# Performance work log

Hardware: AMD Instinct MI355X
Metric: run time of the kernel (lower is better)

## Reference

```python
import jax, jax.numpy as jnp
import numpy as np

N_IN, N_OUT, N_HID = 4, 3, 64
N = N_OUT + N_HID  # 67 neurons (outputs first, matching neuron_key2idx ordering)
H, W = 1024, 1024


def setup_inputs() -> dict:
    key = jax.random.key(0)
    ks = jax.random.split(key, 6)
    inputs = jax.random.normal(ks[0], (H, W, N_IN), jnp.float32)
    # sparse NEAT connectivity encoded as masked dense matrices
    m_in = (jax.random.uniform(ks[1], (N_IN, N)) < 0.5).astype(jnp.float32)
    m_rec = (jax.random.uniform(ks[2], (N, N)) < 0.25).astype(jnp.float32)
    W_in = jax.random.normal(ks[3], (N_IN, N), jnp.float32) * m_in
    W_rec = jax.random.normal(ks[4], (N, N), jnp.float32) * 0.3 * m_rec
    bias = jax.random.normal(ks[5], (N,), jnp.float32) * 0.1
    response = jnp.ones((N,), jnp.float32)
    # neurons with no incoming connections output exactly 0 (original code path)
    has_in = ((m_in.sum(0) + m_rec.sum(0)) > 0).astype(jnp.float32)
    return {"inputs": inputs, "W_in": W_in, "W_rec": W_rec, "bias": bias,
            "response": response, "has_in": has_in, "n_passes": 2}


def reference(inputs, W_in, W_rec, bias, response, has_in, n_passes):
    lead = inputs.shape[:-1]
    x = inputs.reshape(-1, inputs.shape[-1])  # [B, N_IN]
    activs = jnp.zeros((x.shape[0], bias.shape[0]), x.dtype)  # [B, N]
    for _ in range(n_passes):  # small fixed recurrent pass count
        # sum-aggregation of weighted incoming edges from inputs and prev activs
        agg = x @ W_in + activs @ W_rec  # [B, N]
        activs = has_in * jnp.tanh(bias + response * agg)
    out = activs[:, :N_OUT]
    return out.reshape(lead + (N_OUT,))
```

## Files before the change

### kernel.cpp

```cpp
#include <hip/hip_runtime.h>

#define NN   67
#define NOUT 3
#define NIN  4
#define PKW  16
#define PK_FLOATS (NN * PKW)
#define PK_BYTES  (PK_FLOATS * 4)
#define C2   2.885390081777927f

typedef float v2f __attribute__((ext_vector_type(2)));

__device__ __forceinline__ v2f vfma(v2f a, v2f b, v2f c) {
    return __builtin_elementwise_fma(a, b, c);
}

__device__ __forceinline__ float fexp2(float x) {
    float r; asm("v_exp_f32 %0, %1" : "=v"(r) : "v"(x)); return r;
}
__device__ __forceinline__ float frcp(float x) {
    float r; asm("v_rcp_f32 %0, %1" : "=v"(r) : "v"(x)); return r;
}

__device__ __forceinline__ float tanh_sc(float arg) {
    float e = fexp2(arg);
    float r = frcp(e + 1.0f);
    return __builtin_fmaf(-2.0f, r, 1.0f);
}

__global__ void pack_kernel(const float* __restrict__ Win,
                            const float* __restrict__ Wrec,
                            const float* __restrict__ bias,
                            const float* __restrict__ resp,
                            const float* __restrict__ hasin,
                            float* __restrict__ pk)
{
    int j = threadIdx.x;
    if (j < NN) {
        float h = hasin[j];
        float* p = pk + j * PKW;
        p[0] = Win[0*NN + j]; p[1] = Win[1*NN + j];
        p[2] = Win[2*NN + j]; p[3] = Win[3*NN + j];
        p[4] = resp[j] * h * C2;
        p[5] = bias[j] * h * C2;
        p[6] = Wrec[j*NN + 0]; p[7] = Wrec[j*NN + 1]; p[8] = Wrec[j*NN + 2];
        p[9]=p[10]=p[11]=p[12]=p[13]=p[14]=p[15] = 0.f;
    }
}

template<int P>
__global__ __launch_bounds__(256)
void rnn_fused(const float* __restrict__ inputs,
               const float* __restrict__ pk,
               const float* __restrict__ Wrec,
               const int*   __restrict__ np_ptr,
               float*       __restrict__ out,
               int total)
{
    static_assert(P % 2 == 0, "P must be even");
    constexpr int NC = P / 2;

    __shared__ __align__(16) float spk[PK_FLOATS];
    {
        float4*       d = reinterpret_cast<float4*>(spk);
        const float4* s = reinterpret_cast<const float4*>(pk);
        #pragma unroll
        for (int t = 0; t < (PK_FLOATS/4 + 255) / 256; ++t) {
            int i = threadIdx.x + t * 256;
            if (i < PK_FLOATS / 4) d[i] = s[i];
        }
    }
    __syncthreads();

    const int np   = np_ptr[0];
    const int base = blockIdx.x * (256 * P) + threadIdx.x;

    int    pix[P];
    float4 x[P];
#pragma unroll
    for (int p = 0; p < P; ++p) {
        pix[p] = base + p * 256;
        int idx = pix[p] < total ? pix[p] : total - 1;
        x[p] = reinterpret_cast<const float4*>(inputs)[idx];
    }

    float res[P][NOUT];

    if (np == 2) {
        v2f xf[NIN][NC];
#pragma unroll
        for (int c = 0; c < NC; ++c) {
            xf[0][c] = v2f{x[2*c].x, x[2*c+1].x};
            xf[1][c] = v2f{x[2*c].y, x[2*c+1].y};
            xf[2][c] = v2f{x[2*c].z, x[2*c+1].z};
            xf[3][c] = v2f{x[2*c].w, x[2*c+1].w};
        }

        v2f acc[NOUT][NC];
#pragma unroll
        for (int o = 0; o < NOUT; ++o) {
            const float* q = &spk[o * PKW];
            const v2f w0 = {q[0], q[0]}, w1 = {q[1], q[1]},
                      w2 = {q[2], q[2]}, w3 = {q[3], q[3]};
#pragma unroll
            for (int c = 0; c < NC; ++c) {
                v2f a = xf[0][c] * w0;
                a = vfma(xf[1][c], w1, a);
                a = vfma(xf[2][c], w2, a);
                a = vfma(xf[3][c], w3, a);
                acc[o][c] = a;
            }
        }

#pragma unroll
        for (int j = 0; j < NN; ++j) {
            const float* q = &spk[j * PKW];
            const float4 qa = *reinterpret_cast<const float4*>(q);
            const float4 qb = *reinterpret_cast<const float4*>(q + 4);
            const float  wr2s = q[8];
            const v2f w0  = {qa.x, qa.x}, w1 = {qa.y, qa.y},
                      w2  = {qa.z, qa.z}, w3 = {qa.w, qa.w};
            const v2f r2  = {qb.x, qb.x}, b2 = {qb.y, qb.y};
            const v2f wr0 = {qb.z, qb.z}, wr1 = {qb.w, qb.w}, wr2 = {wr2s, wr2s};
#pragma unroll
            for (int c = 0; c < NC; ++c) {
                v2f agg = xf[0][c] * w0;
                agg = vfma(xf[1][c], w1, agg);
                agg = vfma(xf[2][c], w2, agg);
                agg = vfma(xf[3][c], w3, agg);
                v2f arg = vfma(r2, agg, b2);
                v2f a = v2f{tanh_sc(arg.x), tanh_sc(arg.y)};
                acc[0][c] = vfma(a, wr0, acc[0][c]);
                acc[1][c] = vfma(a, wr1, acc[1][c]);
                acc[2][c] = vfma(a, wr2, acc[2][c]);
            }
        }

#pragma unroll
        for (int o = 0; o < NOUT; ++o) {
            const float* q = &spk[o * PKW];
            const float r2s = q[4], b2s = q[5];
#pragma unroll
            for (int c = 0; c < NC; ++c) {
                res[2*c  ][o] = tanh_sc(__builtin_fmaf(r2s, acc[o][c].x, b2s));
                res[2*c+1][o] = tanh_sc(__builtin_fmaf(r2s, acc[o][c].y, b2s));
            }
        }
    } else if (np <= 0) {
#pragma unroll
        for (int p = 0; p < P; ++p)
#pragma unroll
            for (int o = 0; o < NOUT; ++o) res[p][o] = 0.f;
    } else if (np == 1) {
#pragma unroll
        for (int p = 0; p < P; ++p)
#pragma unroll
            for (int o = 0; o < NOUT; ++o) {
                const float* q = &spk[o * PKW];
                float agg = x[p].x * q[0];
                agg = __builtin_fmaf(x[p].y, q[1], agg);
                agg = __builtin_fmaf(x[p].z, q[2], agg);
                agg = __builtin_fmaf(x[p].w, q[3], agg);
                res[p][o] = tanh_sc(__builtin_fmaf(q[4], agg, q[5]));
            }
    } else {
#pragma unroll
        for (int p = 0; p < P; ++p) {
            float act[NN];
            #pragma unroll 1
            for (int j = 0; j < NN; ++j) {
                const float* q = &spk[j * PKW];
                float agg = x[p].x * q[0];
                agg = __builtin_fmaf(x[p].y, q[1], agg);
                agg = __builtin_fmaf(x[p].z, q[2], agg);
                agg = __builtin_fmaf(x[p].w, q[3], agg);
                act[j] = tanh_sc(__builtin_fmaf(q[4], agg, q[5]));
            }
            #pragma unroll 1
            for (int t = 1; t < np - 1; ++t) {
                float na[NN];
                #pragma unroll 1
                for (int j = 0; j < NN; ++j) {
                    const float* q = &spk[j * PKW];
                    float agg = x[p].x * q[0];
                    agg = __builtin_fmaf(x[p].y, q[1], agg);
                    agg = __builtin_fmaf(x[p].z, q[2], agg);
                    agg = __builtin_fmaf(x[p].w, q[3], agg);
                    #pragma unroll 1
                    for (int k = 0; k < NN; ++k)
                        agg = __builtin_fmaf(act[k], Wrec[k*NN + j], agg);
                    na[j] = tanh_sc(__builtin_fmaf(q[4], agg, q[5]));
                }
                #pragma unroll 1
                for (int j = 0; j < NN; ++j) act[j] = na[j];
            }
            #pragma unroll
            for (int o = 0; o < NOUT; ++o) {
                const float* q = &spk[o * PKW];
                float agg = x[p].x * q[0];
                agg = __builtin_fmaf(x[p].y, q[1], agg);
                agg = __builtin_fmaf(x[p].z, q[2], agg);
                agg = __builtin_fmaf(x[p].w, q[3], agg);
                #pragma unroll 1
                for (int k = 0; k < NN; ++k)
                    agg = __builtin_fmaf(act[k], Wrec[k*NN + o], agg);
                res[p][o] = tanh_sc(__builtin_fmaf(q[4], agg, q[5]));
            }
        }
    }

#pragma unroll
    for (int p = 0; p < P; ++p)
        if (pix[p] < total) {
            out[pix[p]*NOUT + 0] = res[p][0];
            out[pix[p]*NOUT + 1] = res[p][1];
            out[pix[p]*NOUT + 2] = res[p][2];
        }
}

__global__ __launch_bounds__(256)
void rnn_general(const float* __restrict__ inputs,
                 const float* __restrict__ Win,
                 const float* __restrict__ Wrec,
                 const float* __restrict__ bias,
                 const float* __restrict__ resp,
                 const float* __restrict__ hasin,
                 const int*   __restrict__ np_ptr,
                 float*       __restrict__ out, int total)
{
    int pix = blockIdx.x * blockDim.x + threadIdx.x;
    if (pix >= total) return;
    const int np = np_ptr[0];
    const float4 x = reinterpret_cast<const float4*>(inputs)[pix];
    float act[NN];
    #pragma unroll 1
    for (int j = 0; j < NN; ++j) act[j] = 0.f;
    #pragma unroll 1
    for (int t = 0; t < np; ++t) {
        float na[NN];
        #pragma unroll 1
        for (int j = 0; j < NN; ++j) {
            float agg = x.x * Win[0*NN+j];
            agg = __builtin_fmaf(x.y, Win[1*NN+j], agg);
            agg = __builtin_fmaf(x.z, Win[2*NN+j], agg);
            agg = __builtin_fmaf(x.w, Win[3*NN+j], agg);
            #pragma unroll 1
            for (int k = 0; k < NN; ++k)
                agg = __builtin_fmaf(act[k], Wrec[k*NN + j], agg);
            na[j] = hasin[j] * tanh_sc(C2 * __builtin_fmaf(resp[j], agg, bias[j]));
        }
        #pragma unroll 1
        for (int j = 0; j < NN; ++j) act[j] = na[j];
    }
    out[pix*NOUT+0] = act[0]; out[pix*NOUT+1] = act[1]; out[pix*NOUT+2] = act[2];
}

extern "C" void kernel_launch(void* const* d_in, const int* in_sizes, int n_in,
                              void* d_out, int out_size, void* d_ws, size_t ws_size,
                              hipStream_t stream) {
    const float* inputs = (const float*)d_in[0];
    const float* Win    = (const float*)d_in[1];
    const float* Wrec   = (const float*)d_in[2];
    const float* bias   = (const float*)d_in[3];
    const float* resp   = (const float*)d_in[4];
    const float* hasin  = (const float*)d_in[5];
    const int*   np     = (const int*)d_in[6];
    float*       out    = (float*)d_out;

    const int total = in_sizes[0] / NIN;

    if (ws_size >= (size_t)PK_BYTES) {
        float* pkbuf = (float*)d_ws;
        pack_kernel<<<1, 128, 0, stream>>>(Win, Wrec, bias, resp, hasin, pkbuf);
        constexpr int P = 4;
        const int block = 256;
        const int grid  = (total + block * P - 1) / (block * P);
        rnn_fused<P><<<grid, block, 0, stream>>>(inputs, pkbuf, Wrec, np, out, total);
    } else {
        const int block = 256;
        const int grid  = (total + block - 1) / block;
        rnn_general<<<grid, block, 0, stream>>>(inputs, Win, Wrec, bias, resp,
                                                hasin, np, out, total);
    }
}
```

Baseline: 103.6 us.

## Fold response scaling into packed weights, shrink table, use P=2 and rolled prefetch loop

The pack kernel now pre-multiplies the input weights by the response and tanh constant, and pre-scales the three output-recurrent weights by the output neurons' scale. This removes the per-neuron response FMA and the final output FMA. The packed row shrinks from 16 to 8 floats with a zero padding row, so each neuron needs two float4 shared loads. The np==2 loop goes from fully unrolled to unroll 4 with a software prefetch of the next row, and pixels per thread drop from 4 to 2, which lowers register pressure but gives less ILP per thread. The general np>2 path now reads the original weights from global memory.

Result: faster. 100.2 us (-3.2%).

```diff
diff --git a/kernel.cpp b/kernel.cpp
--- a/kernel.cpp
+++ b/kernel.cpp
@@ -1,26 +1,25 @@
 #include <hip/hip_runtime.h>
 
-#define NN   67
-#define NOUT 3
-#define NIN  4
-#define PKW  16
-#define PK_FLOATS (NN * PKW)
+#define NN    67
+#define NPAD  68
+#define NOUT  3
+#define NIN   4
+#define PKW8  8
+#define PK_FLOATS (NPAD * PKW8)
 #define PK_BYTES  (PK_FLOATS * 4)
-#define C2   2.885390081777927f
+#define C2 2.885390081777927f
 
 typedef float v2f __attribute__((ext_vector_type(2)));
 
 __device__ __forceinline__ v2f vfma(v2f a, v2f b, v2f c) {
     return __builtin_elementwise_fma(a, b, c);
 }
-
 __device__ __forceinline__ float fexp2(float x) {
     float r; asm("v_exp_f32 %0, %1" : "=v"(r) : "v"(x)); return r;
 }
 __device__ __forceinline__ float frcp(float x) {
     float r; asm("v_rcp_f32 %0, %1" : "=v"(r) : "v"(x)); return r;
 }
-
 __device__ __forceinline__ float tanh_sc(float arg) {
     float e = fexp2(arg);
     float r = frcp(e + 1.0f);
@@ -35,15 +34,25 @@
                             float* __restrict__ pk)
 {
     int j = threadIdx.x;
-    if (j < NN) {
-        float h = hasin[j];
-        float* p = pk + j * PKW;
-        p[0] = Win[0*NN + j]; p[1] = Win[1*NN + j];
-        p[2] = Win[2*NN + j]; p[3] = Win[3*NN + j];
-        p[4] = resp[j] * h * C2;
-        p[5] = bias[j] * h * C2;
-        p[6] = Wrec[j*NN + 0]; p[7] = Wrec[j*NN + 1]; p[8] = Wrec[j*NN + 2];
-        p[9]=p[10]=p[11]=p[12]=p[13]=p[14]=p[15] = 0.f;
+    if (j < NPAD) {
+        float* p = pk + j * PKW8;
+        if (j < NN) {
+            float h  = hasin[j];
+            float r2 = resp[j] * h * C2;
+            p[0] = Win[0*NN + j] * r2;
+            p[1] = Win[1*NN + j] * r2;
+            p[2] = Win[2*NN + j] * r2;
+            p[3] = Win[3*NN + j] * r2;
+            p[4] = bias[j] * h * C2;
+            float r20 = resp[0] * hasin[0] * C2;
+            float r21 = resp[1] * hasin[1] * C2;
+            float r22 = resp[2] * hasin[2] * C2;
+            p[5] = Wrec[j*NN + 0] * r20;
+            p[6] = Wrec[j*NN + 1] * r21;
+            p[7] = Wrec[j*NN + 2] * r22;
+        } else {
+            p[0]=p[1]=p[2]=p[3]=p[4]=p[5]=p[6]=p[7] = 0.f;
+        }
     }
 }
 
@@ -51,23 +60,23 @@
 __global__ __launch_bounds__(256)
 void rnn_fused(const float* __restrict__ inputs,
                const float* __restrict__ pk,
+               const float* __restrict__ Win,
                const float* __restrict__ Wrec,
+               const float* __restrict__ bias,
+               const float* __restrict__ resp,
+               const float* __restrict__ hasin,
                const int*   __restrict__ np_ptr,
                float*       __restrict__ out,
                int total)
 {
-    static_assert(P % 2 == 0, "P must be even");
-    constexpr int NC = P / 2;
+    static_assert(P == 2, "this variant is tuned for P=2");
 
     __shared__ __align__(16) float spk[PK_FLOATS];
     {
         float4*       d = reinterpret_cast<float4*>(spk);
         const float4* s = reinterpret_cast<const float4*>(pk);
-        #pragma unroll
-        for (int t = 0; t < (PK_FLOATS/4 + 255) / 256; ++t) {
-            int i = threadIdx.x + t * 256;
-            if (i < PK_FLOATS / 4) d[i] = s[i];
-        }
+        int i = threadIdx.x;
+        if (i < PK_FLOATS / 4) d[i] = s[i];
     }
     __syncthreads();
 
@@ -85,125 +94,94 @@
 
     float res[P][NOUT];
 
-    if (np == 2) {
-        v2f xf[NIN][NC];
-#pragma unroll
-        for (int c = 0; c < NC; ++c) {
-            xf[0][c] = v2f{x[2*c].x, x[2*c+1].x};
-            xf[1][c] = v2f{x[2*c].y, x[2*c+1].y};
-            xf[2][c] = v2f{x[2*c].z, x[2*c+1].z};
-            xf[3][c] = v2f{x[2*c].w, x[2*c+1].w};
-        }
-
-        v2f acc[NOUT][NC];
+    if (np == 1 || np == 2) {
+        const v2f xf0 = {x[0].x, x[1].x}, xf1 = {x[0].y, x[1].y},
+                  xf2 = {x[0].z, x[1].z}, xf3 = {x[0].w, x[1].w};
+
+        v2f acc[NOUT];
 #pragma unroll
         for (int o = 0; o < NOUT; ++o) {
-            const float* q = &spk[o * PKW];
-            const v2f w0 = {q[0], q[0]}, w1 = {q[1], q[1]},
-                      w2 = {q[2], q[2]}, w3 = {q[3], q[3]};
-#pragma unroll
-            for (int c = 0; c < NC; ++c) {
-                v2f a = xf[0][c] * w0;
-                a = vfma(xf[1][c], w1, a);
-                a = vfma(xf[2][c], w2, a);
-                a = vfma(xf[3][c], w3, a);
-                acc[o][c] = a;
-            }
-        }
-
-#pragma unroll
-        for (int j = 0; j < NN; ++j) {
-            const float* q = &spk[j * PKW];
-            const float4 qa = *reinterpret_cast<const float4*>(q);
-            const float4 qb = *reinterpret_cast<const float4*>(q + 4);
-            const float  wr2s = q[8];
-            const v2f w0  = {qa.x, qa.x}, w1 = {qa.y, qa.y},
-                      w2  = {qa.z, qa.z}, w3 = {qa.w, qa.w};
-            const v2f r2  = {qb.x, qb.x}, b2 = {qb.y, qb.y};
-            const v2f wr0 = {qb.z, qb.z}, wr1 = {qb.w, qb.w}, wr2 = {wr2s, wr2s};
-#pragma unroll
-            for (int c = 0; c < NC; ++c) {
-                v2f agg = xf[0][c] * w0;
-                agg = vfma(xf[1][c], w1, agg);
-                agg = vfma(xf[2][c], w2, agg);
-                agg = vfma(xf[3][c], w3, agg);
-                v2f arg = vfma(r2, agg, b2);
-                v2f a = v2f{tanh_sc(arg.x), tanh_sc(arg.y)};
-                acc[0][c] = vfma(a, wr0, acc[0][c]);
-                acc[1][c] = vfma(a, wr1, acc[1][c]);
-                acc[2][c] = vfma(a, wr2, acc[2][c]);
-            }
-        }
-
+            const float4 qa = *reinterpret_cast<const float4*>(&spk[o * PKW8]);
+            const float  b2 = spk[o * PKW8 + 4];
+            v2f a = {b2, b2};
+            a = vfma(xf0, (v2f){qa.x, qa.x}, a);
+            a = vfma(xf1, (v2f){qa.y, qa.y}, a);
+            a = vfma(xf2, (v2f){qa.z, qa.z}, a);
+            a = vfma(xf3, (v2f){qa.w, qa.w}, a);
+            acc[o] = a;
+        }
+
+        if (np == 2) {
+            float4 qa = *reinterpret_cast<const float4*>(&spk[0]);
+            float4 qb = *reinterpret_cast<const float4*>(&spk[4]);
+#pragma unroll 4
+            for (int j = 0; j < NPAD; ++j) {
+                const int jn = (j + 1 < NPAD) ? j + 1 : NPAD - 1;
+                const float4 qa_n = *reinterpret_cast<const float4*>(&spk[jn * PKW8]);
+                const float4 qb_n = *reinterpret_cast<const float4*>(&spk[jn * PKW8 + 4]);
+
+                v2f arg = {qb.x, qb.x};
+                arg = vfma(xf0, (v2f){qa.x, qa.x}, arg);
+                arg = vfma(xf1, (v2f){qa.y, qa.y}, arg);
+                arg = vfma(xf2, (v2f){qa.z, qa.z}, arg);
+                arg = vfma(xf3, (v2f){qa.w, qa.w}, arg);
+                const v2f a = {tanh_sc(arg.x), tanh_sc(arg.y)};
+                acc[0] = vfma(a, (v2f){qb.y, qb.y}, acc[0]);
+                acc[1] = vfma(a, (v2f){qb.z, qb.z}, acc[1]);
+                acc[2] = vfma(a, (v2f){qb.w, qb.w}, acc[2]);
+
+                qa = qa_n; qb = qb_n;
+            }
+        }
 #pragma unroll
         for (int o = 0; o < NOUT; ++o) {
-            const float* q = &spk[o * PKW];
-            const float r2s = q[4], b2s = q[5];
-#pragma unroll
-            for (int c = 0; c < NC; ++c) {
-                res[2*c  ][o] = tanh_sc(__builtin_fmaf(r2s, acc[o][c].x, b2s));
-                res[2*c+1][o] = tanh_sc(__builtin_fmaf(r2s, acc[o][c].y, b2s));
-            }
+            res[0][o] = tanh_sc(acc[o].x);
+            res[1][o] = tanh_sc(acc[o].y);
         }
     } else if (np <= 0) {
 #pragma unroll
         for (int p = 0; p < P; ++p)
 #pragma unroll
             for (int o = 0; o < NOUT; ++o) res[p][o] = 0.f;
-    } else if (np == 1) {
-#pragma unroll
-        for (int p = 0; p < P; ++p)
-#pragma unroll
-            for (int o = 0; o < NOUT; ++o) {
-                const float* q = &spk[o * PKW];
-                float agg = x[p].x * q[0];
-                agg = __builtin_fmaf(x[p].y, q[1], agg);
-                agg = __builtin_fmaf(x[p].z, q[2], agg);
-                agg = __builtin_fmaf(x[p].w, q[3], agg);
-                res[p][o] = tanh_sc(__builtin_fmaf(q[4], agg, q[5]));
-            }
     } else {
 #pragma unroll
         for (int p = 0; p < P; ++p) {
             float act[NN];
             #pragma unroll 1
             for (int j = 0; j < NN; ++j) {
-                const float* q = &spk[j * PKW];
-                float agg = x[p].x * q[0];
-                agg = __builtin_fmaf(x[p].y, q[1], agg);
-                agg = __builtin_fmaf(x[p].z, q[2], agg);
-                agg = __builtin_fmaf(x[p].w, q[3], agg);
-                act[j] = tanh_sc(__builtin_fmaf(q[4], agg, q[5]));
+                float agg = x[p].x * Win[0*NN+j];
+                agg = __builtin_fmaf(x[p].y, Win[1*NN+j], agg);
+                agg = __builtin_fmaf(x[p].z, Win[2*NN+j], agg);
+                agg = __builtin_fmaf(x[p].w, Win[3*NN+j], agg);
+                act[j] = hasin[j] * tanh_sc(C2 * __builtin_fmaf(resp[j], agg, bias[j]));
             }
             #pragma unroll 1
             for (int t = 1; t < np - 1; ++t) {
                 float na[NN];
                 #pragma unroll 1
                 for (int j = 0; j < NN; ++j) {
-                    const float* q = &spk[j * PKW];
-                    float agg = x[p].x * q[0];
-                    agg = __builtin_fmaf(x[p].y, q[1], agg);
-                    agg = __builtin_fmaf(x[p].z, q[2], agg);
-                    agg = __builtin_fmaf(x[p].w, q[3], agg);
+                    float agg = x[p].x * Win[0*NN+j];
+                    agg = __builtin_fmaf(x[p].y, Win[1*NN+j], agg);
+                    agg = __builtin_fmaf(x[p].z, Win[2*NN+j], agg);
+                    agg = __builtin_fmaf(x[p].w, Win[3*NN+j], agg);
                     #pragma unroll 1
                     for (int k = 0; k < NN; ++k)
                         agg = __builtin_fmaf(act[k], Wrec[k*NN + j], agg);
-                    na[j] = tanh_sc(__builtin_fmaf(q[4], agg, q[5]));
+                    na[j] = hasin[j] * tanh_sc(C2 * __builtin_fmaf(resp[j], agg, bias[j]));
                 }
                 #pragma unroll 1
                 for (int j = 0; j < NN; ++j) act[j] = na[j];
             }
             #pragma unroll
             for (int o = 0; o < NOUT; ++o) {
-                const float* q = &spk[o * PKW];
-                float agg = x[p].x * q[0];
-                agg = __builtin_fmaf(x[p].y, q[1], agg);
-                agg = __builtin_fmaf(x[p].z, q[2], agg);
-                agg = __builtin_fmaf(x[p].w, q[3], agg);
+                float agg = x[p].x * Win[0*NN+o];
+                agg = __builtin_fmaf(x[p].y, Win[1*NN+o], agg);
+                agg = __builtin_fmaf(x[p].z, Win[2*NN+o], agg);
+                agg = __builtin_fmaf(x[p].w, Win[3*NN+o], agg);
                 #pragma unroll 1
                 for (int k = 0; k < NN; ++k)
                     agg = __builtin_fmaf(act[k], Wrec[k*NN + o], agg);
-                res[p][o] = tanh_sc(__builtin_fmaf(q[4], agg, q[5]));
+                res[p][o] = hasin[o] * tanh_sc(C2 * __builtin_fmaf(resp[o], agg, bias[o]));
             }
         }
     }
@@ -271,10 +249,11 @@
     if (ws_size >= (size_t)PK_BYTES) {
         float* pkbuf = (float*)d_ws;
         pack_kernel<<<1, 128, 0, stream>>>(Win, Wrec, bias, resp, hasin, pkbuf);
-        constexpr int P = 4;
+        constexpr int P = 2;
         const int block = 256;
         const int grid  = (total + block * P - 1) / (block * P);
-        rnn_fused<P><<<grid, block, 0, stream>>>(inputs, pkbuf, Wrec, np, out, total);
+        rnn_fused<P><<<grid, block, 0, stream>>>(inputs, pkbuf, Win, Wrec, bias,
+                                                 resp, hasin, np, out, total);
     } else {
         const int block = 256;
         const int grid  = (total + block - 1) / block;
```
